# Kernel optimization log

Hardware: AMD Instinct MI355X
Metric: run time of the kernel (lower is better)

Reference implementation:

```python
import jax, jax.numpy as jnp
import numpy as np

N_QUBITS = 64
N_STATES = 256
BATCH = 1048576


def setup_inputs() -> dict:
    key = jax.random.key(0)
    x = jax.random.randint(key, (BATCH,), 0, 100000, dtype=jnp.int64 if jax.config.jax_enable_x64 else jnp.int32)
    return {"x": x}


def reference(x) -> jnp.ndarray:
    # state = x % n_states; index = state % n_qubits; one-hot over n_qubits.
    idx = (x % N_STATES) % N_QUBITS  # [B]
    basis = jax.nn.one_hot(idx, N_QUBITS, dtype=jnp.float32)  # [B, n_qubits]
    return basis
```

## Files before the change

### kernel.cpp

```cpp
#include <hip/hip_runtime.h>


#define BATCH (1048576)
#define VEC_PER_ROW 16
#define TOTAL_VEC (BATCH * VEC_PER_ROW)

__global__ __launch_bounds__(256) void basis_encoder_kernel(
    const int* __restrict__ x, float4* __restrict__ out) {
  int gid = blockIdx.x * blockDim.x + threadIdx.x;
  int row = gid >> 4;
  int chunk = gid & 15;
  unsigned idx = (unsigned)x[row] & 63u;
  int base = chunk << 2;
  float4 v;
  v.x = (idx == (unsigned)(base + 0)) ? 1.0f : 0.0f;
  v.y = (idx == (unsigned)(base + 1)) ? 1.0f : 0.0f;
  v.z = (idx == (unsigned)(base + 2)) ? 1.0f : 0.0f;
  v.w = (idx == (unsigned)(base + 3)) ? 1.0f : 0.0f;
  out[gid] = v;
}

extern "C" void kernel_launch(void* const* d_in, const int* in_sizes, int n_in,
                              void* d_out, int out_size, void* d_ws, size_t ws_size,
                              hipStream_t stream) {
  const int* x = (const int*)d_in[0];
  float4* out = (float4*)d_out;
  basis_encoder_kernel<<<TOTAL_VEC / 256, 256, 0, stream>>>(x, out);
}
```

Baseline: 268.2 us.

## Use persistent grid-stride loop with unrolled loads and nontemporal vector stores

Replaces the one-thread-per-float4 launch with a fixed grid of 2048 blocks where each thread handles 32 float4 chunks in unrolled batches of 8, issuing all index loads before the stores. Output writes use nontemporal stores to avoid polluting caches on this write-bound 256MB output. The intent is to cut block launch overhead and raise memory-level parallelism; fewer blocks may underfill the device or reduce latency hiding if the fixed grid is too small.

```diff
diff --git a/kernel.cpp b/kernel.cpp
--- a/kernel.cpp
+++ b/kernel.cpp
@@ -1,29 +1,46 @@
 #include <hip/hip_runtime.h>
 
 
+typedef float f32x4 __attribute__((ext_vector_type(4)));
+
 #define BATCH (1048576)
-#define VEC_PER_ROW 16
-#define TOTAL_VEC (BATCH * VEC_PER_ROW)
+#define TOTAL_VEC (BATCH * 16)
 
-__global__ __launch_bounds__(256) void basis_encoder_kernel(
-    const int* __restrict__ x, float4* __restrict__ out) {
-  int gid = blockIdx.x * blockDim.x + threadIdx.x;
-  int row = gid >> 4;
-  int chunk = gid & 15;
-  unsigned idx = (unsigned)x[row] & 63u;
-  int base = chunk << 2;
-  float4 v;
-  v.x = (idx == (unsigned)(base + 0)) ? 1.0f : 0.0f;
-  v.y = (idx == (unsigned)(base + 1)) ? 1.0f : 0.0f;
-  v.z = (idx == (unsigned)(base + 2)) ? 1.0f : 0.0f;
-  v.w = (idx == (unsigned)(base + 3)) ? 1.0f : 0.0f;
-  out[gid] = v;
+constexpr int TPB = 256;
+constexpr int BLOCKS = 2048;
+constexpr int GRID_THREADS = TPB * BLOCKS;
+constexpr int ITERS = TOTAL_VEC / GRID_THREADS;
+constexpr int UNROLL = 8;
+
+__global__ __launch_bounds__(TPB) void basis_encoder_kernel(
+    const int* __restrict__ x, f32x4* __restrict__ out) {
+  const int tid = blockIdx.x * TPB + threadIdx.x;
+  const int base = (tid & 15) << 2;
+  #pragma unroll
+  for (int outer = 0; outer < ITERS / UNROLL; ++outer) {
+    unsigned idx[UNROLL];
+    int gid[UNROLL];
+    #pragma unroll
+    for (int u = 0; u < UNROLL; ++u) {
+      gid[u] = tid + (outer * UNROLL + u) * GRID_THREADS;
+      idx[u] = (unsigned)x[gid[u] >> 4] & 63u;
+    }
+    #pragma unroll
+    for (int u = 0; u < UNROLL; ++u) {
+      f32x4 v;
+      v.x = (idx[u] == (unsigned)(base + 0)) ? 1.0f : 0.0f;
+      v.y = (idx[u] == (unsigned)(base + 1)) ? 1.0f : 0.0f;
+      v.z = (idx[u] == (unsigned)(base + 2)) ? 1.0f : 0.0f;
+      v.w = (idx[u] == (unsigned)(base + 3)) ? 1.0f : 0.0f;
+      __builtin_nontemporal_store(v, &out[gid[u]]);
+    }
+  }
 }
 
 extern "C" void kernel_launch(void* const* d_in, const int* in_sizes, int n_in,
                               void* d_out, int out_size, void* d_ws, size_t ws_size,
                               hipStream_t stream) {
   const int* x = (const int*)d_in[0];
-  float4* out = (float4*)d_out;
-  basis_encoder_kernel<<<TOTAL_VEC / 256, 256, 0, stream>>>(x, out);
+  f32x4* out = (f32x4*)d_out;
+  basis_encoder_kernel<<<BLOCKS, TPB, 0, stream>>>(x, out);
 }
```

New measurement: 274.0 us. 2.1% more time.

## Replace dense one-hot write with memset plus sparse scatter of ones

Applied to the files above, without the earlier changes.

Instead of computing and writing every float4 of the one-hot output in the kernel, the output is zeroed with hipMemsetAsync and a lighter kernel scatters a single 1.0f per row, reading four inputs per thread as an int4 vector. The aim is to offload the bulk zero fill to the runtime's memset path and shrink the compute kernel. The total write traffic is still the full 256 MB, and the scatter adds scattered 4-byte writes and a second launch. Correctness relies on the memset finishing before the scatter on the same stream.

```diff
diff --git a/kernel.cpp b/kernel.cpp
--- a/kernel.cpp
+++ b/kernel.cpp
@@ -2,28 +2,29 @@
 
 
 #define BATCH (1048576)
-#define VEC_PER_ROW 16
-#define TOTAL_VEC (BATCH * VEC_PER_ROW)
 
-__global__ __launch_bounds__(256) void basis_encoder_kernel(
-    const int* __restrict__ x, float4* __restrict__ out) {
-  int gid = blockIdx.x * blockDim.x + threadIdx.x;
-  int row = gid >> 4;
-  int chunk = gid & 15;
-  unsigned idx = (unsigned)x[row] & 63u;
-  int base = chunk << 2;
-  float4 v;
-  v.x = (idx == (unsigned)(base + 0)) ? 1.0f : 0.0f;
-  v.y = (idx == (unsigned)(base + 1)) ? 1.0f : 0.0f;
-  v.z = (idx == (unsigned)(base + 2)) ? 1.0f : 0.0f;
-  v.w = (idx == (unsigned)(base + 3)) ? 1.0f : 0.0f;
-  out[gid] = v;
+constexpr int TPB = 256;
+constexpr int ROWS_PER_THREAD = 4;
+constexpr int BLOCKS = BATCH / (TPB * ROWS_PER_THREAD);
+
+typedef int i32x4 __attribute__((ext_vector_type(4)));
+
+__global__ __launch_bounds__(TPB) void basis_scatter_kernel(
+    const i32x4* __restrict__ x4, float* __restrict__ out) {
+  int t = blockIdx.x * TPB + threadIdx.x;
+  i32x4 xv = x4[t];
+  int row0 = t * 4;
+  out[(size_t)(row0 + 0) * 64 + (xv.x & 63)] = 1.0f;
+  out[(size_t)(row0 + 1) * 64 + (xv.y & 63)] = 1.0f;
+  out[(size_t)(row0 + 2) * 64 + (xv.z & 63)] = 1.0f;
+  out[(size_t)(row0 + 3) * 64 + (xv.w & 63)] = 1.0f;
 }
 
 extern "C" void kernel_launch(void* const* d_in, const int* in_sizes, int n_in,
                               void* d_out, int out_size, void* d_ws, size_t ws_size,
                               hipStream_t stream) {
-  const int* x = (const int*)d_in[0];
-  float4* out = (float4*)d_out;
-  basis_encoder_kernel<<<TOTAL_VEC / 256, 256, 0, stream>>>(x, out);
+  const i32x4* x4 = (const i32x4*)d_in[0];
+  float* out = (float*)d_out;
+  hipMemsetAsync(d_out, 0, (size_t)out_size * sizeof(float), stream);
+  basis_scatter_kernel<<<BLOCKS, TPB, 0, stream>>>(x4, out);
 }
```

Result: slower. 280.9 us (+4.7%).
